# Kernel optimization log

Hardware: AMD Instinct MI355X
Metric: run time of the kernel (lower is better)

The kernel has to match this reference:

```python
import jax, jax.numpy as jnp
import numpy as np

B, L, D, H, NL = 32, 200, 64, 2, 2
ITEM_NUM, TIME_SPAN = 50000, 365
NEG = float(-2**32 + 1)


def _ln(x, g, b, eps=1e-8):
    m = jnp.mean(x, -1, keepdims=True)
    v = jnp.mean((x - m) ** 2, -1, keepdims=True)
    return (x - m) / jnp.sqrt(v + eps) * g + b


def setup_inputs() -> dict:
    key = jax.random.key(0)
    ks = iter(jax.random.split(key, 32))
    f = lambda shape: jax.random.normal(next(ks), shape, jnp.float32) * 0.02
    item_emb = f((ITEM_NUM + 1, D)).at[0].set(0.0)  # padding_idx=0
    return dict(
        log_ids=jax.random.randint(next(ks), (B, L), 0, ITEM_NUM + 1),
        log_times=jax.random.randint(next(ks), (B, L), 0, 100_000_000),
        pos_ids=jax.random.randint(next(ks), (B, L), 1, ITEM_NUM + 1),
        neg_ids=jax.random.randint(next(ks), (B, L), 1, ITEM_NUM + 1),
        item_emb=item_emb,
        posK_emb=f((L, D)), posV_emb=f((L, D)),
        tK_emb=f((TIME_SPAN + 1, D)), tV_emb=f((TIME_SPAN + 1, D)),
        ln1_g=jnp.ones((NL, D)), ln1_b=jnp.zeros((NL, D)),
        Wq=f((NL, D, D)), bq=jnp.zeros((NL, D)),
        Wk=f((NL, D, D)), bk=jnp.zeros((NL, D)),
        Wv=f((NL, D, D)), bv=jnp.zeros((NL, D)),
        ln2_g=jnp.ones((NL, D)), ln2_b=jnp.zeros((NL, D)),
        W1=f((NL, D, D)), b1=jnp.zeros((NL, D)),
        W2=f((NL, D, D)), b2=jnp.zeros((NL, D)),
        lnf_g=jnp.ones((D,)), lnf_b=jnp.zeros((D,)),
    )


def _attention(xq, xkv, pad, cmask, tK, tV, pK, pV, Wq, bq, Wk, bk, Wv, bv):
    dh = D // H
    Q = xq @ Wq.T + bq
    K = xkv @ Wk.T + bk
    V = xkv @ Wv.T + bv
    heads = lambda t: t.reshape(B, L, H, dh).transpose(2, 0, 1, 3)  # [H,B,L,dh]
    Qh, Kh, Vh = heads(Q), heads(K), heads(V)
    pKh = pK.reshape(L, H, dh).transpose(1, 0, 2)  # [H,L,dh] (same for all b)
    pVh = pV.reshape(L, H, dh).transpose(1, 0, 2)
    tKh = tK.reshape(B, L, L, H, dh).transpose(3, 0, 1, 2, 4)  # [H,B,Lq,Lk,dh]
    tVh = tV.reshape(B, L, L, H, dh).transpose(3, 0, 1, 2, 4)
    s = jnp.einsum('hbqd,hbkd->hbqk', Qh, Kh)
    s = s + jnp.einsum('hbqd,hkd->hbqk', Qh, pKh)
    s = s + jnp.einsum('hbqkd,hbqd->hbqk', tKh, Qh)
    s = s / (dh ** 0.5)
    s = jnp.where(pad[None, :, :, None], NEG, s)  # padded query rows
    s = jnp.where(cmask[None, None, :, :], NEG, s)  # causal mask
    A = jax.nn.softmax(s, axis=-1)
    out = jnp.einsum('hbqk,hbkd->hbqd', A, Vh)
    out = out + jnp.einsum('hbqk,hkd->hbqd', A, pVh)
    out = out + jnp.einsum('hbqk,hbqkd->hbqd', A, tVh)
    return out.transpose(1, 2, 0, 3).reshape(B, L, D)


def reference(log_ids, log_times, pos_ids, neg_ids, item_emb, posK_emb, posV_emb,
              tK_emb, tV_emb, ln1_g, ln1_b, Wq, bq, Wk, bk, Wv, bv,
              ln2_g, ln2_b, W1, b1, W2, b2, lnf_g, lnf_b):
    # per-pair time-interval buckets (days, clipped to TIME_SPAN)
    dt = jnp.abs(log_times[:, :, None] - log_times[:, None, :]).astype(jnp.float32) / 86400.0
    tmat = jnp.minimum(dt, TIME_SPAN).astype(jnp.int32)
    tK = tK_emb[tmat]  # [B,L,L,D]
    tV = tV_emb[tmat]
    pad = (log_ids == 0)
    keep = (~pad)[:, :, None].astype(item_emb.dtype)
    cmask = ~jnp.tril(jnp.ones((L, L), dtype=bool))
    x = item_emb[log_ids] * (D ** 0.5) * keep
    for i in range(NL):
        q = _ln(x, ln1_g[i], ln1_b[i])
        mha = _attention(q, x, pad, cmask, tK, tV, posK_emb, posV_emb,
                         Wq[i], bq[i], Wk[i], bk[i], Wv[i], bv[i])
        x = q + mha
        x = _ln(x, ln2_g[i], ln2_b[i])
        x = x + (jax.nn.relu(x @ W1[i].T + b1[i]) @ W2[i].T + b2[i])  # 1x1 conv FFN
        x = x * keep
    feats = _ln(x, lnf_g, lnf_b)
    pos_logits = jnp.sum(feats * item_emb[pos_ids], -1)
    neg_logits = jnp.sum(feats * item_emb[neg_ids], -1)
    return pos_logits, neg_logits
```

## Files before the change

kernel.cpp:

```cpp
#include <hip/hip_runtime.h>
#include <math.h>

#define BB 32
#define LLEN 200
#define DD 64
#define HH 2
#define NLAYER 2
#define BLD (BB * LLEN * DD)
#define TSPAN1 366

__device__ inline float waveSum(float v) {
#pragma unroll
    for (int off = 32; off > 0; off >>= 1) v += __shfl_xor(v, off);
    return v;
}
__device__ inline float halfSum(float v) {
    v += __shfl_xor(v, 1);
    v += __shfl_xor(v, 2);
    v += __shfl_xor(v, 4);
    v += __shfl_xor(v, 8);
    v += __shfl_xor(v, 16);
    return v;
}
__device__ inline float halfMax(float v) {
    v = fmaxf(v, __shfl_xor(v, 1));
    v = fmaxf(v, __shfl_xor(v, 2));
    v = fmaxf(v, __shfl_xor(v, 4));
    v = fmaxf(v, __shfl_xor(v, 8));
    v = fmaxf(v, __shfl_xor(v, 16));
    return v;
}

__global__ void transpose_kernel(const float* __restrict__ Wq,
                                 const float* __restrict__ Wk,
                                 const float* __restrict__ Wv,
                                 const float* __restrict__ W1,
                                 const float* __restrict__ W2,
                                 const float* __restrict__ tK_emb,
                                 float* __restrict__ wt,
                                 float* __restrict__ tKT) {
    int m = blockIdx.x;
    if (m < 10) {
        const float* src;
        switch (m % 5) {
            case 0: src = Wq; break;
            case 1: src = Wk; break;
            case 2: src = Wv; break;
            case 3: src = W1; break;
            default: src = W2; break;
        }
        src += (m / 5) * DD * DD;
        float* dst = wt + m * DD * DD;
        for (int e = threadIdx.x; e < DD * DD; e += 256) {
            int d = e >> 6, j = e & 63;
            dst[j * DD + d] = src[e];
        }
    } else {
        for (int e = threadIdx.x; e < TSPAN1 * DD; e += 256) {
            int t = e >> 6, d = e & 63;
            tKT[d * TSPAN1 + t] = tK_emb[e];
        }
    }
}

__global__ void ln_qkv_kernel(const int* __restrict__ log_ids,
                              const float* __restrict__ item_emb,
                              const float* __restrict__ g,
                              const float* __restrict__ bln,
                              const float* __restrict__ WqT, const float* __restrict__ bq,
                              const float* __restrict__ WkT, const float* __restrict__ bk,
                              const float* __restrict__ WvT, const float* __restrict__ bv,
                              const float* __restrict__ posK,
                              const float* __restrict__ posV,
                              float* __restrict__ q,
                              float* __restrict__ Q, float* __restrict__ K,
                              float* __restrict__ V) {
    __shared__ float qs[4][DD], xs[4][DD];
    int tid = threadIdx.x;
    int wid = tid >> 6, d = tid & 63;
    int row = blockIdx.x * 4 + wid;
    int l = row % LLEN;
    int id = log_ids[row];
    float xv = (id == 0) ? 0.0f : item_emb[id * DD + d] * 8.0f;
    xs[wid][d] = xv;
    float m = waveSum(xv) * (1.0f / 64.0f);
    float c = xv - m;
    float var = waveSum(c * c) * (1.0f / 64.0f);
    float qv = (c / sqrtf(var + 1e-8f)) * g[d] + bln[d];
    qs[wid][d] = qv;
    q[row * DD + d] = qv;
    float aq = bq[d], ak = bk[d], av = bv[d];
#pragma unroll 8
    for (int j = 0; j < DD; ++j) {
        aq = fmaf(qs[wid][j], WqT[j * DD + d], aq);
        ak = fmaf(xs[wid][j], WkT[j * DD + d], ak);
        av = fmaf(xs[wid][j], WvT[j * DD + d], av);
    }
    Q[row * DD + d] = aq;
    K[row * DD + d] = ak + posK[l * DD + d];
    V[row * DD + d] = av + posV[l * DD + d];
}

__global__ void qt_kernel(const float* __restrict__ Q,
                          const float* __restrict__ tKT,
                          float* __restrict__ Qt_g) {
    __shared__ float Qs[16][DD];
    int tid = threadIdx.x;
    int base = blockIdx.x * 16;
    for (int e = tid; e < 16 * DD; e += 384)
        Qs[e >> 6][e & 63] = Q[(base + (e >> 6)) * DD + (e & 63)];
    __syncthreads();
    int t = tid;
    if (t < TSPAN1) {
        float acc[16];
#pragma unroll
        for (int gg = 0; gg < 16; ++gg) acc[gg] = 0.0f;
        for (int d = 0; d < 32; ++d) {
            float v = tKT[d * TSPAN1 + t];
#pragma unroll
            for (int gg = 0; gg < 16; ++gg) acc[gg] = fmaf(v, Qs[gg][d], acc[gg]);
        }
#pragma unroll
        for (int gg = 0; gg < 16; ++gg)
            Qt_g[(base + gg) * (2 * TSPAN1) + t] = acc[gg];
#pragma unroll
        for (int gg = 0; gg < 16; ++gg) acc[gg] = 0.0f;
        for (int d = 32; d < 64; ++d) {
            float v = tKT[d * TSPAN1 + t];
#pragma unroll
            for (int gg = 0; gg < 16; ++gg) acc[gg] = fmaf(v, Qs[gg][d], acc[gg]);
        }
#pragma unroll
        for (int gg = 0; gg < 16; ++gg)
            Qt_g[(base + gg) * (2 * TSPAN1) + TSPAN1 + t] = acc[gg];
    }
}

__global__ void attn_kernel(const float* __restrict__ Q,
                            const float* __restrict__ Keff,
                            const float* __restrict__ Veff,
                            const int* __restrict__ log_times,
                            const float* __restrict__ Qt_g,
                            const float* __restrict__ tV_emb,
                            float* __restrict__ out) {
    __shared__ int t_s[LLEN];
    __shared__ float sc[4][HH][LLEN];
    __shared__ unsigned short tm_s[4][LLEN];

    int tid = threadIdx.x;
    int wid = tid >> 6;
    int lane = tid & 63;
    int bi = blockIdx.x / 50;
    int i = blockIdx.x % 50;
    int qi = (wid == 0) ? i : (wid == 1) ? (99 - i) : (wid == 2) ? (100 + i) : (199 - i);
    int row = bi * LLEN + qi;
    int len = qi + 1;

    if (tid < LLEN) t_s[tid] = log_times[bi * LLEN + tid];
    __syncthreads();

    int tq = t_s[qi];
    for (int k = lane; k < len; k += 64) {
        int dt = tq - t_s[k];
        if (dt < 0) dt = -dt;
        float dtf = fminf((float)dt * (1.0f / 86400.0f), 365.0f);
        tm_s[wid][k] = (unsigned short)(int)dtf;
    }

    int h = lane >> 5;
    int l5 = lane & 31;
    int cch = l5 >> 2;
    int jo = l5 & 3;
    float4 qv = ((const float4*)(Q + row * DD))[h * 8 + cch];
    const float4* K4 = (const float4*)(Keff + bi * LLEN * DD);
    const float* qtrow = Qt_g + row * (2 * TSPAN1) + h * TSPAN1;
    const float scale = 0.17677669529663687f;

    for (int k0 = 0; k0 < len; k0 += 4) {
        int k = k0 + jo;
        int kc = (k < len) ? k : (len - 1);
        int bucket = tm_s[wid][kc];
        float4 kv = K4[kc * 16 + h * 8 + cch];
        float p = qv.x * kv.x + qv.y * kv.y + qv.z * kv.z + qv.w * kv.w;
        p += __shfl_xor(p, 4);
        p += __shfl_xor(p, 8);
        p += __shfl_xor(p, 16);
        float s = (p + qtrow[bucket]) * scale;
        if (cch == 0 && k < len) sc[wid][h][k] = s;
    }

    {
        float m = -INFINITY;
        for (int k = l5; k < len; k += 32) m = fmaxf(m, sc[wid][h][k]);
        m = halfMax(m);
        float s = 0.0f;
        for (int k = l5; k < len; k += 32) {
            float e = expf(sc[wid][h][k] - m);
            sc[wid][h][k] = e;
            s += e;
        }
        s = halfSum(s);
        float inv = 1.0f / s;
        for (int k = l5; k < len; k += 32) sc[wid][h][k] *= inv;
    }

    const float* Vb = Veff + bi * LLEN * DD + lane;
    const float* tVl = tV_emb + lane;
    float acc0 = 0.0f, acc1 = 0.0f, acc2 = 0.0f, acc3 = 0.0f;
    int k = 0;
    for (; k + 4 <= len; k += 4) {
        int b0 = tm_s[wid][k + 0];
        int b1 = tm_s[wid][k + 1];
        int b2 = tm_s[wid][k + 2];
        int b3 = tm_s[wid][k + 3];
        float a0 = sc[wid][h][k + 0];
        float a1 = sc[wid][h][k + 1];
        float a2 = sc[wid][h][k + 2];
        float a3 = sc[wid][h][k + 3];
        acc0 = fmaf(a0, Vb[(k + 0) * DD] + tVl[b0 * DD], acc0);
        acc1 = fmaf(a1, Vb[(k + 1) * DD] + tVl[b1 * DD], acc1);
        acc2 = fmaf(a2, Vb[(k + 2) * DD] + tVl[b2 * DD], acc2);
        acc3 = fmaf(a3, Vb[(k + 3) * DD] + tVl[b3 * DD], acc3);
    }
    for (; k < len; ++k) {
        int b0 = tm_s[wid][k];
        acc0 = fmaf(sc[wid][h][k], Vb[k * DD] + tVl[b0 * DD], acc0);
    }
    out[row * DD + lane] = (acc0 + acc1) + (acc2 + acc3);
}

__global__ void mid_kernel(const float* __restrict__ qin,
                           const float* __restrict__ att,
                           const float* __restrict__ g2, const float* __restrict__ b2ln,
                           const float* __restrict__ W1T, const float* __restrict__ b1v,
                           const float* __restrict__ W2T, const float* __restrict__ b2v,
                           const int* __restrict__ log_ids,
                           const float* __restrict__ g1n, const float* __restrict__ b1n,
                           const float* __restrict__ WqT, const float* __restrict__ bq,
                           const float* __restrict__ WkT, const float* __restrict__ bk,
                           const float* __restrict__ WvT, const float* __restrict__ bv,
                           const float* __restrict__ posK,
                           const float* __restrict__ posV,
                           float* __restrict__ q,
                           float* __restrict__ Q, float* __restrict__ K,
                           float* __restrict__ V) {
    __shared__ float xs[4][DD], hs[4][DD], qs[4][DD];
    int tid = threadIdx.x;
    int wid = tid >> 6, d = tid & 63;
    int row = blockIdx.x * 4 + wid;
    int l = row % LLEN;
    float v = qin[row * DD + d] + att[row * DD + d];
    float m = waveSum(v) * (1.0f / 64.0f);
    float c = v - m;
    float var = waveSum(c * c) * (1.0f / 64.0f);
    float xv = (c / sqrtf(var + 1e-8f)) * g2[d] + b2ln[d];
    xs[wid][d] = xv;
    float a = b1v[d];
#pragma unroll 8
    for (int j = 0; j < DD; ++j) a = fmaf(xs[wid][j], W1T[j * DD + d], a);
    hs[wid][d] = fmaxf(a, 0.0f);
    float o = b2v[d];
#pragma unroll 8
    for (int j = 0; j < DD; ++j) o = fmaf(hs[wid][j], W2T[j * DD + d], o);
    float res = xv + o;
    if (log_ids[row] == 0) res = 0.0f;
    float m2 = waveSum(res) * (1.0f / 64.0f);
    float c2 = res - m2;
    float var2 = waveSum(c2 * c2) * (1.0f / 64.0f);
    float qv = (c2 / sqrtf(var2 + 1e-8f)) * g1n[d] + b1n[d];
    qs[wid][d] = qv;
    xs[wid][d] = res;
    q[row * DD + d] = qv;
    float aq = bq[d], ak = bk[d], av = bv[d];
#pragma unroll 8
    for (int j = 0; j < DD; ++j) {
        aq = fmaf(qs[wid][j], WqT[j * DD + d], aq);
        ak = fmaf(xs[wid][j], WkT[j * DD + d], ak);
        av = fmaf(xs[wid][j], WvT[j * DD + d], av);
    }
    Q[row * DD + d] = aq;
    K[row * DD + d] = ak + posK[l * DD + d];
    V[row * DD + d] = av + posV[l * DD + d];
}

__global__ void end_kernel(const float* __restrict__ qin,
                           const float* __restrict__ att,
                           const float* __restrict__ g2, const float* __restrict__ b2ln,
                           const float* __restrict__ W1T, const float* __restrict__ b1v,
                           const float* __restrict__ W2T, const float* __restrict__ b2v,
                           const int* __restrict__ log_ids,
                           const float* __restrict__ lnf_g, const float* __restrict__ lnf_b,
                           const float* __restrict__ item_emb,
                           const int* __restrict__ pos_ids,
                           const int* __restrict__ neg_ids,
                           float* __restrict__ out) {
    __shared__ float xs[4][DD], hs[4][DD];
    int tid = threadIdx.x;
    int wid = tid >> 6, d = tid & 63;
    int row = blockIdx.x * 4 + wid;
    float v = qin[row * DD + d] + att[row * DD + d];
    float m = waveSum(v) * (1.0f / 64.0f);
    float c = v - m;
    float var = waveSum(c * c) * (1.0f / 64.0f);
    float xv = (c / sqrtf(var + 1e-8f)) * g2[d] + b2ln[d];
    xs[wid][d] = xv;
    float a = b1v[d];
#pragma unroll 8
    for (int j = 0; j < DD; ++j) a = fmaf(xs[wid][j], W1T[j * DD + d], a);
    hs[wid][d] = fmaxf(a, 0.0f);
    float o = b2v[d];
#pragma unroll 8
    for (int j = 0; j < DD; ++j) o = fmaf(hs[wid][j], W2T[j * DD + d], o);
    float res = xv + o;
    if (log_ids[row] == 0) res = 0.0f;
    float m2 = waveSum(res) * (1.0f / 64.0f);
    float c2 = res - m2;
    float var2 = waveSum(c2 * c2) * (1.0f / 64.0f);
    float f = (c2 / sqrtf(var2 + 1e-8f)) * lnf_g[d] + lnf_b[d];
    int pid = pos_ids[row];
    int nid = neg_ids[row];
    float p = waveSum(f * item_emb[pid * DD + d]);
    float n = waveSum(f * item_emb[nid * DD + d]);
    if (d == 0) {
        out[row] = p;
        out[BB * LLEN + row] = n;
    }
}

extern "C" void kernel_launch(void* const* d_in, const int* in_sizes, int n_in,
                              void* d_out, int out_size, void* d_ws, size_t ws_size,
                              hipStream_t stream) {
    const int* log_ids = (const int*)d_in[0];
    const int* log_times = (const int*)d_in[1];
    const int* pos_ids = (const int*)d_in[2];
    const int* neg_ids = (const int*)d_in[3];
    const float* item_emb = (const float*)d_in[4];
    const float* posK = (const float*)d_in[5];
    const float* posV = (const float*)d_in[6];
    const float* tK_emb = (const float*)d_in[7];
    const float* tV_emb = (const float*)d_in[8];
    const float* ln1_g = (const float*)d_in[9];
    const float* ln1_b = (const float*)d_in[10];
    const float* Wq = (const float*)d_in[11];
    const float* bq = (const float*)d_in[12];
    const float* Wk = (const float*)d_in[13];
    const float* bk = (const float*)d_in[14];
    const float* Wv = (const float*)d_in[15];
    const float* bv = (const float*)d_in[16];
    const float* ln2_g = (const float*)d_in[17];
    const float* ln2_b = (const float*)d_in[18];
    const float* W1 = (const float*)d_in[19];
    const float* b1 = (const float*)d_in[20];
    const float* W2 = (const float*)d_in[21];
    const float* b2 = (const float*)d_in[22];
    const float* lnf_g = (const float*)d_in[23];
    const float* lnf_b = (const float*)d_in[24];

    float* ws = (float*)d_ws;
    float* q = ws;
    float* Qb = q + BLD;
    float* Kb = Qb + BLD;
    float* Vb = Kb + BLD;
    float* att = Vb + BLD;
    float* wt = att + BLD;
    float* tKT = wt + 10 * DD * DD;
    float* Qt = tKT + DD * TSPAN1;

    const int nrow = BB * LLEN;

    const float* W1T0 = wt + 3 * DD * DD;
    const float* W2T0 = wt + 4 * DD * DD;
    const float* W1T1 = wt + 8 * DD * DD;
    const float* W2T1 = wt + 9 * DD * DD;

    transpose_kernel<<<11, 256, 0, stream>>>(Wq, Wk, Wv, W1, W2, tK_emb, wt, tKT);

    ln_qkv_kernel<<<nrow / 4, 256, 0, stream>>>(log_ids, item_emb,
                                                ln1_g, ln1_b,
                                                wt + 0 * DD * DD, bq,
                                                wt + 1 * DD * DD, bk,
                                                wt + 2 * DD * DD, bv,
                                                posK, posV,
                                                q, Qb, Kb, Vb);
    qt_kernel<<<nrow / 16, 384, 0, stream>>>(Qb, tKT, Qt);
    attn_kernel<<<BB * 50, 256, 0, stream>>>(Qb, Kb, Vb, log_times, Qt, tV_emb, att);

    mid_kernel<<<nrow / 4, 256, 0, stream>>>(q, att,
                                             ln2_g, ln2_b,
                                             W1T0, b1, W2T0, b2,
                                             log_ids,
                                             ln1_g + DD, ln1_b + DD,
                                             wt + 5 * DD * DD, bq + DD,
                                             wt + 6 * DD * DD, bk + DD,
                                             wt + 7 * DD * DD, bv + DD,
                                             posK, posV,
                                             q, Qb, Kb, Vb);
    qt_kernel<<<nrow / 16, 384, 0, stream>>>(Qb, tKT, Qt);
    attn_kernel<<<BB * 50, 256, 0, stream>>>(Qb, Kb, Vb, log_times, Qt, tV_emb, att);

    end_kernel<<<nrow / 4, 256, 0, stream>>>(q, att,
                                             ln2_g + DD, ln2_b + DD,
                                             W1T1, b1 + DD, W2T1, b2 + DD,
                                             log_ids,
                                             lnf_g, lnf_b, item_emb,
                                             pos_ids, neg_ids, (float*)d_out);
}
```

Baseline: 198.4 us.

## Split attention keys across two waves per query with flash-style merge

Each attention block now handles two query rows, with two waves per row that each cover half of the key range. Each half keeps its own running max and sum, and the partials are merged after a block barrier using the usual log-sum-exp rescaling. The Qt bucket rows are staged into shared memory instead of being gathered from global memory. This doubles the grid and shortens each wave's serial key loop, at the cost of more shared memory, an extra barrier and the merge step.

Result: no change. 197.3 us (-0.5%).

```diff
diff --git a/kernel.cpp b/kernel.cpp
--- a/kernel.cpp
+++ b/kernel.cpp
@@ -144,27 +144,41 @@
                             const float* __restrict__ tV_emb,
                             float* __restrict__ out) {
     __shared__ int t_s[LLEN];
-    __shared__ float sc[4][HH][LLEN];
-    __shared__ unsigned short tm_s[4][LLEN];
+    __shared__ float qt_s[2][2 * TSPAN1];
+    __shared__ float sc[2][HH][LLEN];
+    __shared__ unsigned short tm_s[2][LLEN];
+    __shared__ float o_l[2][2][DD];
+    __shared__ float ml_l[2][2][HH][2];
 
     int tid = threadIdx.x;
     int wid = tid >> 6;
     int lane = tid & 63;
-    int bi = blockIdx.x / 50;
-    int i = blockIdx.x % 50;
-    int qi = (wid == 0) ? i : (wid == 1) ? (99 - i) : (wid == 2) ? (100 + i) : (199 - i);
-    int row = bi * LLEN + qi;
-    int len = qi + 1;
+    int bi = blockIdx.x / 100;
+    int i = blockIdx.x % 100;
+    int qsel = wid >> 1, half = wid & 1;
+    int qa = i, qb = 199 - i;
+    int rowa = bi * LLEN + qa, rowb = bi * LLEN + qb;
+    int qq = qsel ? qb : qa;
+    int row = qsel ? rowb : rowa;
+    int len = qq + 1;
+    int mid = (((len + 1) >> 1) + 3) & ~3;
+    if (mid > len) mid = len;
+    int k_lo = half ? mid : 0;
+    int k_hi = half ? len : mid;
 
     if (tid < LLEN) t_s[tid] = log_times[bi * LLEN + tid];
+    for (int e = tid; e < 2 * 2 * TSPAN1; e += 256) {
+        int qs_ = (e >= 2 * TSPAN1);
+        int c = e - qs_ * 2 * TSPAN1;
+        qt_s[qs_][c] = Qt_g[(qs_ ? rowb : rowa) * (2 * TSPAN1) + c];
+    }
     __syncthreads();
 
-    int tq = t_s[qi];
-    for (int k = lane; k < len; k += 64) {
+    int tq = t_s[qq];
+    for (int k = k_lo + lane; k < k_hi; k += 64) {
         int dt = tq - t_s[k];
         if (dt < 0) dt = -dt;
-        float dtf = fminf((float)dt * (1.0f / 86400.0f), 365.0f);
-        tm_s[wid][k] = (unsigned short)(int)dtf;
+        tm_s[qsel][k] = (unsigned short)(int)fminf((float)dt * (1.0f / 86400.0f), 365.0f);
     }
 
     int h = lane >> 5;
@@ -173,60 +187,75 @@
     int jo = l5 & 3;
     float4 qv = ((const float4*)(Q + row * DD))[h * 8 + cch];
     const float4* K4 = (const float4*)(Keff + bi * LLEN * DD);
-    const float* qtrow = Qt_g + row * (2 * TSPAN1) + h * TSPAN1;
+    const float* qtrow = &qt_s[qsel][h * TSPAN1];
     const float scale = 0.17677669529663687f;
 
-    for (int k0 = 0; k0 < len; k0 += 4) {
+    for (int k0 = k_lo; k0 < k_hi; k0 += 4) {
         int k = k0 + jo;
-        int kc = (k < len) ? k : (len - 1);
-        int bucket = tm_s[wid][kc];
+        int kc = (k < k_hi) ? k : (k_hi - 1);
+        int bucket = tm_s[qsel][kc];
         float4 kv = K4[kc * 16 + h * 8 + cch];
         float p = qv.x * kv.x + qv.y * kv.y + qv.z * kv.z + qv.w * kv.w;
         p += __shfl_xor(p, 4);
         p += __shfl_xor(p, 8);
         p += __shfl_xor(p, 16);
         float s = (p + qtrow[bucket]) * scale;
-        if (cch == 0 && k < len) sc[wid][h][k] = s;
-    }
-
-    {
-        float m = -INFINITY;
-        for (int k = l5; k < len; k += 32) m = fmaxf(m, sc[wid][h][k]);
-        m = halfMax(m);
-        float s = 0.0f;
-        for (int k = l5; k < len; k += 32) {
-            float e = expf(sc[wid][h][k] - m);
-            sc[wid][h][k] = e;
-            s += e;
-        }
-        s = halfSum(s);
-        float inv = 1.0f / s;
-        for (int k = l5; k < len; k += 32) sc[wid][h][k] *= inv;
-    }
+        if (cch == 0 && k < k_hi) sc[qsel][h][k] = s;
+    }
+
+    float mloc = -INFINITY;
+    for (int k = k_lo + l5; k < k_hi; k += 32) mloc = fmaxf(mloc, sc[qsel][h][k]);
+    mloc = halfMax(mloc);
+    float lloc = 0.0f;
+    for (int k = k_lo + l5; k < k_hi; k += 32) {
+        float e = expf(sc[qsel][h][k] - mloc);
+        sc[qsel][h][k] = e;
+        lloc += e;
+    }
+    lloc = halfSum(lloc);
 
     const float* Vb = Veff + bi * LLEN * DD + lane;
     const float* tVl = tV_emb + lane;
     float acc0 = 0.0f, acc1 = 0.0f, acc2 = 0.0f, acc3 = 0.0f;
-    int k = 0;
-    for (; k + 4 <= len; k += 4) {
-        int b0 = tm_s[wid][k + 0];
-        int b1 = tm_s[wid][k + 1];
-        int b2 = tm_s[wid][k + 2];
-        int b3 = tm_s[wid][k + 3];
-        float a0 = sc[wid][h][k + 0];
-        float a1 = sc[wid][h][k + 1];
-        float a2 = sc[wid][h][k + 2];
-        float a3 = sc[wid][h][k + 3];
+    int k = k_lo;
+    for (; k + 4 <= k_hi; k += 4) {
+        int b0 = tm_s[qsel][k + 0];
+        int b1 = tm_s[qsel][k + 1];
+        int b2 = tm_s[qsel][k + 2];
+        int b3 = tm_s[qsel][k + 3];
+        float a0 = sc[qsel][h][k + 0];
+        float a1 = sc[qsel][h][k + 1];
+        float a2 = sc[qsel][h][k + 2];
+        float a3 = sc[qsel][h][k + 3];
         acc0 = fmaf(a0, Vb[(k + 0) * DD] + tVl[b0 * DD], acc0);
         acc1 = fmaf(a1, Vb[(k + 1) * DD] + tVl[b1 * DD], acc1);
         acc2 = fmaf(a2, Vb[(k + 2) * DD] + tVl[b2 * DD], acc2);
         acc3 = fmaf(a3, Vb[(k + 3) * DD] + tVl[b3 * DD], acc3);
     }
-    for (; k < len; ++k) {
-        int b0 = tm_s[wid][k];
-        acc0 = fmaf(sc[wid][h][k], Vb[k * DD] + tVl[b0 * DD], acc0);
-    }
-    out[row * DD + lane] = (acc0 + acc1) + (acc2 + acc3);
+    for (; k < k_hi; ++k) {
+        int b0 = tm_s[qsel][k];
+        acc0 = fmaf(sc[qsel][h][k], Vb[k * DD] + tVl[b0 * DD], acc0);
+    }
+    o_l[qsel][half][lane] = (acc0 + acc1) + (acc2 + acc3);
+    if (l5 == 0) {
+        ml_l[qsel][half][h][0] = mloc;
+        ml_l[qsel][half][h][1] = lloc;
+    }
+    __syncthreads();
+
+    if (wid < 2) {
+        int qs_ = wid;
+        int r = qs_ ? rowb : rowa;
+        int hh = lane >> 5;
+        float m0 = ml_l[qs_][0][hh][0], l0 = ml_l[qs_][0][hh][1];
+        float m1 = ml_l[qs_][1][hh][0], l1 = ml_l[qs_][1][hh][1];
+        float M = fmaxf(m0, m1);
+        float a0 = expf(m0 - M);
+        float a1 = expf(m1 - M);
+        float L = a0 * l0 + a1 * l1;
+        float o = a0 * o_l[qs_][0][lane] + a1 * o_l[qs_][1][lane];
+        out[r * DD + lane] = o / L;
+    }
 }
 
 __global__ void mid_kernel(const float* __restrict__ qin,
@@ -383,7 +412,7 @@
                                                 posK, posV,
                                                 q, Qb, Kb, Vb);
     qt_kernel<<<nrow / 16, 384, 0, stream>>>(Qb, tKT, Qt);
-    attn_kernel<<<BB * 50, 256, 0, stream>>>(Qb, Kb, Vb, log_times, Qt, tV_emb, att);
+    attn_kernel<<<BB * 100, 256, 0, stream>>>(Qb, Kb, Vb, log_times, Qt, tV_emb, att);
 
     mid_kernel<<<nrow / 4, 256, 0, stream>>>(q, att,
                                              ln2_g, ln2_b,
@@ -396,7 +425,7 @@
                                              posK, posV,
                                              q, Qb, Kb, Vb);
     qt_kernel<<<nrow / 16, 384, 0, stream>>>(Qb, tKT, Qt);
-    attn_kernel<<<BB * 50, 256, 0, stream>>>(Qb, Kb, Vb, log_times, Qt, tV_emb, att);
+    attn_kernel<<<BB * 100, 256, 0, stream>>>(Qb, Kb, Vb, log_times, Qt, tV_emb, att);
 
     end_kernel<<<nrow / 4, 256, 0, stream>>>(q, att,
                                              ln2_g + DD, ln2_b + DD,
```

## Fuse Q·tK bucket projection into attention kernel using shared memory

Applied to the files above, without the earlier changes.

Removes the separate qt_kernel and computes the per-query projection of Q onto all time-interval key embeddings inside the attention kernel, storing it in shared memory instead of a global buffer. Blocks now handle 8 consecutive queries with 512 threads instead of 4 load-balanced queries with 256 threads. This saves a launch and a global write/read of the Qt buffer per layer, but drops the causal load-balancing pairing and raises shared memory use per block, which may reduce occupancy.

Result: slower. 210.6 us (+6.2%).

```diff
diff --git a/kernel.cpp b/kernel.cpp
--- a/kernel.cpp
+++ b/kernel.cpp
@@ -101,107 +101,100 @@
     V[row * DD + d] = av + posV[l * DD + d];
 }
 
-__global__ void qt_kernel(const float* __restrict__ Q,
-                          const float* __restrict__ tKT,
-                          float* __restrict__ Qt_g) {
-    __shared__ float Qs[16][DD];
+__global__ void __launch_bounds__(512, 6)
+attn_kernel(const float* __restrict__ Q,
+            const float* __restrict__ Keff,
+            const float* __restrict__ Veff,
+            const int* __restrict__ log_times,
+            const float* __restrict__ tKT,
+            const float* __restrict__ tV_emb,
+            float* __restrict__ out) {
+    __shared__ int t_s[LLEN];
+    __shared__ float Qs[8][DD];
+    __shared__ float qt_s[8][2 * TSPAN1];
+    __shared__ float sc[8][HH][LLEN];
+    __shared__ unsigned short tm_s[8][LLEN];
+
     int tid = threadIdx.x;
-    int base = blockIdx.x * 16;
-    for (int e = tid; e < 16 * DD; e += 384)
-        Qs[e >> 6][e & 63] = Q[(base + (e >> 6)) * DD + (e & 63)];
-    __syncthreads();
-    int t = tid;
-    if (t < TSPAN1) {
-        float acc[16];
-#pragma unroll
-        for (int gg = 0; gg < 16; ++gg) acc[gg] = 0.0f;
-        for (int d = 0; d < 32; ++d) {
-            float v = tKT[d * TSPAN1 + t];
-#pragma unroll
-            for (int gg = 0; gg < 16; ++gg) acc[gg] = fmaf(v, Qs[gg][d], acc[gg]);
-        }
-#pragma unroll
-        for (int gg = 0; gg < 16; ++gg)
-            Qt_g[(base + gg) * (2 * TSPAN1) + t] = acc[gg];
-#pragma unroll
-        for (int gg = 0; gg < 16; ++gg) acc[gg] = 0.0f;
-        for (int d = 32; d < 64; ++d) {
-            float v = tKT[d * TSPAN1 + t];
-#pragma unroll
-            for (int gg = 0; gg < 16; ++gg) acc[gg] = fmaf(v, Qs[gg][d], acc[gg]);
-        }
-#pragma unroll
-        for (int gg = 0; gg < 16; ++gg)
-            Qt_g[(base + gg) * (2 * TSPAN1) + TSPAN1 + t] = acc[gg];
-    }
-}
-
-__global__ void attn_kernel(const float* __restrict__ Q,
-                            const float* __restrict__ Keff,
-                            const float* __restrict__ Veff,
-                            const int* __restrict__ log_times,
-                            const float* __restrict__ Qt_g,
-                            const float* __restrict__ tV_emb,
-                            float* __restrict__ out) {
-    __shared__ int t_s[LLEN];
-    __shared__ float sc[4][HH][LLEN];
-    __shared__ unsigned short tm_s[4][LLEN];
-
-    int tid = threadIdx.x;
-    int wid = tid >> 6;
+    int w = tid >> 6;
     int lane = tid & 63;
-    int bi = blockIdx.x / 50;
-    int i = blockIdx.x % 50;
-    int qi = (wid == 0) ? i : (wid == 1) ? (99 - i) : (wid == 2) ? (100 + i) : (199 - i);
+    int bi = blockIdx.x / 25;
+    int t8 = blockIdx.x % 25;
+    int qi = t8 * 8 + w;
     int row = bi * LLEN + qi;
     int len = qi + 1;
 
     if (tid < LLEN) t_s[tid] = log_times[bi * LLEN + tid];
+    Qs[w][lane] = Q[row * DD + lane];
     __syncthreads();
 
     int tq = t_s[qi];
     for (int k = lane; k < len; k += 64) {
         int dt = tq - t_s[k];
         if (dt < 0) dt = -dt;
-        float dtf = fminf((float)dt * (1.0f / 86400.0f), 365.0f);
-        tm_s[wid][k] = (unsigned short)(int)dtf;
-    }
+        tm_s[w][k] = (unsigned short)(int)fminf((float)dt * (1.0f / 86400.0f), 365.0f);
+    }
+
+    for (int u = w; u < 12; u += 8) {
+        int chunk = u >> 1, h = u & 1;
+        int tt = chunk * 64 + lane;
+        if (tt < TSPAN1) {
+            float a0 = 0, a1 = 0, a2 = 0, a3 = 0, a4 = 0, a5 = 0, a6 = 0, a7 = 0;
+            const float* tk = tKT + (h * 32) * TSPAN1 + tt;
+            const float* qsh = &Qs[0][h * 32];
+            for (int d = 0; d < 32; ++d) {
+                float v = tk[d * TSPAN1];
+                a0 = fmaf(v, qsh[0 * DD + d], a0);
+                a1 = fmaf(v, qsh[1 * DD + d], a1);
+                a2 = fmaf(v, qsh[2 * DD + d], a2);
+                a3 = fmaf(v, qsh[3 * DD + d], a3);
+                a4 = fmaf(v, qsh[4 * DD + d], a4);
+                a5 = fmaf(v, qsh[5 * DD + d], a5);
+                a6 = fmaf(v, qsh[6 * DD + d], a6);
+                a7 = fmaf(v, qsh[7 * DD + d], a7);
+            }
+            int o = h * TSPAN1 + tt;
+            qt_s[0][o] = a0; qt_s[1][o] = a1; qt_s[2][o] = a2; qt_s[3][o] = a3;
+            qt_s[4][o] = a4; qt_s[5][o] = a5; qt_s[6][o] = a6; qt_s[7][o] = a7;
+        }
+    }
+    __syncthreads();
 
     int h = lane >> 5;
     int l5 = lane & 31;
     int cch = l5 >> 2;
     int jo = l5 & 3;
-    float4 qv = ((const float4*)(Q + row * DD))[h * 8 + cch];
+    float4 qv = ((const float4*)(&Qs[w][0]))[h * 8 + cch];
     const float4* K4 = (const float4*)(Keff + bi * LLEN * DD);
-    const float* qtrow = Qt_g + row * (2 * TSPAN1) + h * TSPAN1;
+    const float* qtrow = &qt_s[w][h * TSPAN1];
     const float scale = 0.17677669529663687f;
 
     for (int k0 = 0; k0 < len; k0 += 4) {
         int k = k0 + jo;
         int kc = (k < len) ? k : (len - 1);
-        int bucket = tm_s[wid][kc];
+        int bucket = tm_s[w][kc];
         float4 kv = K4[kc * 16 + h * 8 + cch];
         float p = qv.x * kv.x + qv.y * kv.y + qv.z * kv.z + qv.w * kv.w;
         p += __shfl_xor(p, 4);
         p += __shfl_xor(p, 8);
         p += __shfl_xor(p, 16);
         float s = (p + qtrow[bucket]) * scale;
-        if (cch == 0 && k < len) sc[wid][h][k] = s;
+        if (cch == 0 && k < len) sc[w][h][k] = s;
     }
 
     {
         float m = -INFINITY;
-        for (int k = l5; k < len; k += 32) m = fmaxf(m, sc[wid][h][k]);
+        for (int k = l5; k < len; k += 32) m = fmaxf(m, sc[w][h][k]);
         m = halfMax(m);
         float s = 0.0f;
         for (int k = l5; k < len; k += 32) {
-            float e = expf(sc[wid][h][k] - m);
-            sc[wid][h][k] = e;
+            float e = expf(sc[w][h][k] - m);
+            sc[w][h][k] = e;
             s += e;
         }
         s = halfSum(s);
         float inv = 1.0f / s;
-        for (int k = l5; k < len; k += 32) sc[wid][h][k] *= inv;
+        for (int k = l5; k < len; k += 32) sc[w][h][k] *= inv;
     }
 
     const float* Vb = Veff + bi * LLEN * DD + lane;
@@ -209,22 +202,22 @@
     float acc0 = 0.0f, acc1 = 0.0f, acc2 = 0.0f, acc3 = 0.0f;
     int k = 0;
     for (; k + 4 <= len; k += 4) {
-        int b0 = tm_s[wid][k + 0];
-        int b1 = tm_s[wid][k + 1];
-        int b2 = tm_s[wid][k + 2];
-        int b3 = tm_s[wid][k + 3];
-        float a0 = sc[wid][h][k + 0];
-        float a1 = sc[wid][h][k + 1];
-        float a2 = sc[wid][h][k + 2];
-        float a3 = sc[wid][h][k + 3];
+        int b0 = tm_s[w][k + 0];
+        int b1 = tm_s[w][k + 1];
+        int b2 = tm_s[w][k + 2];
+        int b3 = tm_s[w][k + 3];
+        float a0 = sc[w][h][k + 0];
+        float a1 = sc[w][h][k + 1];
+        float a2 = sc[w][h][k + 2];
+        float a3 = sc[w][h][k + 3];
         acc0 = fmaf(a0, Vb[(k + 0) * DD] + tVl[b0 * DD], acc0);
         acc1 = fmaf(a1, Vb[(k + 1) * DD] + tVl[b1 * DD], acc1);
         acc2 = fmaf(a2, Vb[(k + 2) * DD] + tVl[b2 * DD], acc2);
         acc3 = fmaf(a3, Vb[(k + 3) * DD] + tVl[b3 * DD], acc3);
     }
     for (; k < len; ++k) {
-        int b0 = tm_s[wid][k];
-        acc0 = fmaf(sc[wid][h][k], Vb[k * DD] + tVl[b0 * DD], acc0);
+        int b0 = tm_s[w][k];
+        acc0 = fmaf(sc[w][h][k], Vb[k * DD] + tVl[b0 * DD], acc0);
     }
     out[row * DD + lane] = (acc0 + acc1) + (acc2 + acc3);
 }
@@ -364,7 +357,6 @@
     float* att = Vb + BLD;
     float* wt = att + BLD;
     float* tKT = wt + 10 * DD * DD;
-    float* Qt = tKT + DD * TSPAN1;
 
     const int nrow = BB * LLEN;
 
@@ -382,8 +374,7 @@
                                                 wt + 2 * DD * DD, bv,
                                                 posK, posV,
                                                 q, Qb, Kb, Vb);
-    qt_kernel<<<nrow / 16, 384, 0, stream>>>(Qb, tKT, Qt);
-    attn_kernel<<<BB * 50, 256, 0, stream>>>(Qb, Kb, Vb, log_times, Qt, tV_emb, att);
+    attn_kernel<<<BB * 25, 512, 0, stream>>>(Qb, Kb, Vb, log_times, tKT, tV_emb, att);
 
     mid_kernel<<<nrow / 4, 256, 0, stream>>>(q, att,
                                              ln2_g, ln2_b,
@@ -395,8 +386,7 @@
                                              wt + 7 * DD * DD, bv + DD,
                                              posK, posV,
                                              q, Qb, Kb, Vb);
-    qt_kernel<<<nrow / 16, 384, 0, stream>>>(Qb, tKT, Qt);
-    attn_kernel<<<BB * 50, 256, 0, stream>>>(Qb, Kb, Vb, log_times, Qt, tV_emb, att);
+    attn_kernel<<<BB * 25, 512, 0, stream>>>(Qb, Kb, Vb, log_times, tKT, tV_emb, att);
 
     end_kernel<<<nrow / 4, 256, 0, stream>>>(q, att,
                                              ln2_g + DD, ln2_b + DD,
```

## Fuse Q·tK projection into QKV kernels and stage Qt rows in shared memory

Applied to the files above, without the earlier changes.

Removes the separate qt_kernel launches by computing the per-row Q·tK bucket table at the end of the LN/QKV and mid kernels, using the freshly computed Q kept in shared memory. Each block now handles 4 rows instead of 16, so tKT is re-read four times as often, with less reuse per load. The attention kernel also copies each query's 732-entry Qt row into shared memory before scoring, replacing scattered global gathers with LDS lookups at the cost of more shared memory per block.

Measured after the change: 183.3 us. -7.6%, faster.

```diff
diff --git a/kernel.cpp b/kernel.cpp
--- a/kernel.cpp
+++ b/kernel.cpp
@@ -29,6 +29,40 @@
     v = fmaxf(v, __shfl_xor(v, 8));
     v = fmaxf(v, __shfl_xor(v, 16));
     return v;
+}
+
+__device__ inline void qt_tail(const float (*Qsh)[DD], const float* __restrict__ tKT,
+                               float* __restrict__ Qt_g, int base) {
+    int tid = threadIdx.x;
+    for (int t = tid; t < TSPAN1; t += 256) {
+        const float* tk = tKT + t;
+        float a0 = 0, a1 = 0, a2 = 0, a3 = 0;
+#pragma unroll 8
+        for (int d = 0; d < 32; ++d) {
+            float v = tk[d * TSPAN1];
+            a0 = fmaf(v, Qsh[0][d], a0);
+            a1 = fmaf(v, Qsh[1][d], a1);
+            a2 = fmaf(v, Qsh[2][d], a2);
+            a3 = fmaf(v, Qsh[3][d], a3);
+        }
+        Qt_g[(base + 0) * (2 * TSPAN1) + t] = a0;
+        Qt_g[(base + 1) * (2 * TSPAN1) + t] = a1;
+        Qt_g[(base + 2) * (2 * TSPAN1) + t] = a2;
+        Qt_g[(base + 3) * (2 * TSPAN1) + t] = a3;
+        float b0 = 0, b1 = 0, b2 = 0, b3 = 0;
+#pragma unroll 8
+        for (int d = 32; d < 64; ++d) {
+            float v = tk[d * TSPAN1];
+            b0 = fmaf(v, Qsh[0][d], b0);
+            b1 = fmaf(v, Qsh[1][d], b1);
+            b2 = fmaf(v, Qsh[2][d], b2);
+            b3 = fmaf(v, Qsh[3][d], b3);
+        }
+        Qt_g[(base + 0) * (2 * TSPAN1) + TSPAN1 + t] = b0;
+        Qt_g[(base + 1) * (2 * TSPAN1) + TSPAN1 + t] = b1;
+        Qt_g[(base + 2) * (2 * TSPAN1) + TSPAN1 + t] = b2;
+        Qt_g[(base + 3) * (2 * TSPAN1) + TSPAN1 + t] = b3;
+    }
 }
 
 __global__ void transpose_kernel(const float* __restrict__ Wq,
@@ -72,10 +106,12 @@
                               const float* __restrict__ WvT, const float* __restrict__ bv,
                               const float* __restrict__ posK,
                               const float* __restrict__ posV,
+                              const float* __restrict__ tKT,
                               float* __restrict__ q,
                               float* __restrict__ Q, float* __restrict__ K,
-                              float* __restrict__ V) {
-    __shared__ float qs[4][DD], xs[4][DD];
+                              float* __restrict__ V,
+                              float* __restrict__ Qt_g) {
+    __shared__ float qs[4][DD], xs[4][DD], Qsh[4][DD];
     int tid = threadIdx.x;
     int wid = tid >> 6, d = tid & 63;
     int row = blockIdx.x * 4 + wid;
@@ -99,41 +135,9 @@
     Q[row * DD + d] = aq;
     K[row * DD + d] = ak + posK[l * DD + d];
     V[row * DD + d] = av + posV[l * DD + d];
-}
-
-__global__ void qt_kernel(const float* __restrict__ Q,
-                          const float* __restrict__ tKT,
-                          float* __restrict__ Qt_g) {
-    __shared__ float Qs[16][DD];
-    int tid = threadIdx.x;
-    int base = blockIdx.x * 16;
-    for (int e = tid; e < 16 * DD; e += 384)
-        Qs[e >> 6][e & 63] = Q[(base + (e >> 6)) * DD + (e & 63)];
+    Qsh[wid][d] = aq;
     __syncthreads();
-    int t = tid;
-    if (t < TSPAN1) {
-        float acc[16];
-#pragma unroll
-        for (int gg = 0; gg < 16; ++gg) acc[gg] = 0.0f;
-        for (int d = 0; d < 32; ++d) {
-            float v = tKT[d * TSPAN1 + t];
-#pragma unroll
-            for (int gg = 0; gg < 16; ++gg) acc[gg] = fmaf(v, Qs[gg][d], acc[gg]);
-        }
-#pragma unroll
-        for (int gg = 0; gg < 16; ++gg)
-            Qt_g[(base + gg) * (2 * TSPAN1) + t] = acc[gg];
-#pragma unroll
-        for (int gg = 0; gg < 16; ++gg) acc[gg] = 0.0f;
-        for (int d = 32; d < 64; ++d) {
-            float v = tKT[d * TSPAN1 + t];
-#pragma unroll
-            for (int gg = 0; gg < 16; ++gg) acc[gg] = fmaf(v, Qs[gg][d], acc[gg]);
-        }
-#pragma unroll
-        for (int gg = 0; gg < 16; ++gg)
-            Qt_g[(base + gg) * (2 * TSPAN1) + TSPAN1 + t] = acc[gg];
-    }
+    qt_tail(Qsh, tKT, Qt_g, blockIdx.x * 4);
 }
 
 __global__ void attn_kernel(const float* __restrict__ Q,
@@ -146,6 +150,7 @@
     __shared__ int t_s[LLEN];
     __shared__ float sc[4][HH][LLEN];
     __shared__ unsigned short tm_s[4][LLEN];
+    __shared__ float qt_s[4][2 * TSPAN1];
 
     int tid = threadIdx.x;
     int wid = tid >> 6;
@@ -159,6 +164,9 @@
     if (tid < LLEN) t_s[tid] = log_times[bi * LLEN + tid];
     __syncthreads();
 
+    const float* qtrow_g = Qt_g + row * (2 * TSPAN1);
+    for (int e = lane; e < 2 * TSPAN1; e += 64) qt_s[wid][e] = qtrow_g[e];
+
     int tq = t_s[qi];
     for (int k = lane; k < len; k += 64) {
         int dt = tq - t_s[k];
@@ -173,7 +181,6 @@
     int jo = l5 & 3;
     float4 qv = ((const float4*)(Q + row * DD))[h * 8 + cch];
     const float4* K4 = (const float4*)(Keff + bi * LLEN * DD);
-    const float* qtrow = Qt_g + row * (2 * TSPAN1) + h * TSPAN1;
     const float scale = 0.17677669529663687f;
 
     for (int k0 = 0; k0 < len; k0 += 4) {
@@ -185,7 +192,7 @@
         p += __shfl_xor(p, 4);
         p += __shfl_xor(p, 8);
         p += __shfl_xor(p, 16);
-        float s = (p + qtrow[bucket]) * scale;
+        float s = (p + qt_s[wid][h * TSPAN1 + bucket]) * scale;
         if (cch == 0 && k < len) sc[wid][h][k] = s;
     }
 
@@ -241,10 +248,12 @@
                            const float* __restrict__ WvT, const float* __restrict__ bv,
                            const float* __restrict__ posK,
                            const float* __restrict__ posV,
+                           const float* __restrict__ tKT,
                            float* __restrict__ q,
                            float* __restrict__ Q, float* __restrict__ K,
-                           float* __restrict__ V) {
-    __shared__ float xs[4][DD], hs[4][DD], qs[4][DD];
+                           float* __restrict__ V,
+                           float* __restrict__ Qt_g) {
+    __shared__ float xs[4][DD], hs[4][DD], qs[4][DD], Qsh[4][DD];
     int tid = threadIdx.x;
     int wid = tid >> 6, d = tid & 63;
     int row = blockIdx.x * 4 + wid;
@@ -281,6 +290,9 @@
     Q[row * DD + d] = aq;
     K[row * DD + d] = ak + posK[l * DD + d];
     V[row * DD + d] = av + posV[l * DD + d];
+    Qsh[wid][d] = aq;
+    __syncthreads();
+    qt_tail(Qsh, tKT, Qt_g, blockIdx.x * 4);
 }
 
 __global__ void end_kernel(const float* __restrict__ qin,
@@ -380,9 +392,8 @@
                                                 wt + 0 * DD * DD, bq,
                                                 wt + 1 * DD * DD, bk,
                                                 wt + 2 * DD * DD, bv,
-                                                posK, posV,
-                                                q, Qb, Kb, Vb);
-    qt_kernel<<<nrow / 16, 384, 0, stream>>>(Qb, tKT, Qt);
+                                                posK, posV, tKT,
+                                                q, Qb, Kb, Vb, Qt);
     attn_kernel<<<BB * 50, 256, 0, stream>>>(Qb, Kb, Vb, log_times, Qt, tV_emb, att);
 
     mid_kernel<<<nrow / 4, 256, 0, stream>>>(q, att,
@@ -393,9 +404,8 @@
                                              wt + 5 * DD * DD, bq + DD,
                                              wt + 6 * DD * DD, bk + DD,
                                              wt + 7 * DD * DD, bv + DD,
-                                             posK, posV,
-                                             q, Qb, Kb, Vb);
-    qt_kernel<<<nrow / 16, 384, 0, stream>>>(Qb, tKT, Qt);
+                                             posK, posV, tKT,
+                                             q, Qb, Kb, Vb, Qt);
     attn_kernel<<<BB * 50, 256, 0, stream>>>(Qb, Kb, Vb, log_times, Qt, tV_emb, att);
 
     end_kernel<<<nrow / 4, 256, 0, stream>>>(q, att,
```
